# Kernel tuning notes

Measured on AMD Instinct MI355X. Metric: run time of the kernel, lower is better.

Reference implementation:

```python
import jax, jax.numpy as jnp
import numpy as np

N_NODES = 50000
N_EDGES = 800000
IN_CH = 128
HID_CH = 128
OUT_CH = 64
N_GRAPHS = 256


def setup_inputs() -> dict:
    key = jax.random.key(0)
    k1, k2, k3, k4, k5, k6, k7 = jax.random.split(key, 7)
    x = jax.random.normal(k1, (N_NODES, IN_CH), dtype=jnp.float32)
    edge_index = jax.random.randint(k2, (2, N_EDGES), 0, N_NODES, dtype=jnp.int64)
    batch = jnp.sort(jax.random.randint(k3, (N_NODES,), 0, N_GRAPHS, dtype=jnp.int64))
    # GCNConv params (glorot-ish scale) and Linear params
    W1 = jax.random.normal(k4, (IN_CH, HID_CH), dtype=jnp.float32) / np.sqrt(IN_CH)
    b1 = jnp.zeros((HID_CH,), dtype=jnp.float32)
    W2 = jax.random.normal(k5, (HID_CH, OUT_CH), dtype=jnp.float32) / np.sqrt(HID_CH)
    b2 = jax.random.normal(k6, (OUT_CH,), dtype=jnp.float32) * 0.01
    return {"x": x, "edge_index": edge_index, "batch": batch,
            "W1": W1, "b1": b1, "W2": W2, "b2": b2}


def _gcn_conv(x, edge_index, W, b):
    # PyG GCNConv: add self loops, symmetric normalization, linear transform,
    # gather-scale-scatter aggregation, bias.
    n = x.shape[0]
    loop = jnp.arange(n, dtype=edge_index.dtype)
    src = jnp.concatenate([edge_index[0], loop])  # message sources
    dst = jnp.concatenate([edge_index[1], loop])  # aggregation targets
    deg = jax.ops.segment_sum(jnp.ones_like(dst, dtype=x.dtype), dst, num_segments=n)
    dinv = jnp.where(deg > 0, jax.lax.rsqrt(deg), 0.0)
    norm = dinv[src] * dinv[dst]                  # [E+N]
    h = x @ W                                     # [N, hid] transform first (in >= hid)
    msg = h[src] * norm[:, None]                  # [E+N, hid] gather + scale
    agg = jax.ops.segment_sum(msg, dst, num_segments=n)  # scatter-add
    return agg + b


def reference(x, edge_index, batch, W1, b1, W2, b2):
    h = _gcn_conv(x, edge_index, W1, b1)
    h = jax.nn.relu(h)
    # dropout is identity in eval mode
    pooled = jax.ops.segment_max(h, batch, num_segments=N_GRAPHS)  # global max pool
    pooled = jnp.where(jnp.isfinite(pooled), pooled, 0.0)          # empty graphs -> 0
    out = jax.nn.relu(pooled @ W2 + b2)
    return out
```

## Files before the change

### kernel.cpp

```cpp
#include <hip/hip_runtime.h>

#define NN 50000
#define NE 800000
#define NG 256
#define NB 256
#define BW 196
#define NBIN 200
#define EPB 4000
#define PAD 16
#define CAP 4608
#define WT_STRIDE 136

typedef __attribute__((ext_vector_type(8))) short bf16x8;
typedef __attribute__((ext_vector_type(4))) float f32x4;
typedef __attribute__((ext_vector_type(2))) float f32x2;

static __device__ __forceinline__ unsigned short f2b(float f) {
    unsigned int u = __float_as_uint(f);
    return (unsigned short)((u + 0x7FFFu + ((u >> 16) & 1u)) >> 16);
}
static __device__ __forceinline__ unsigned char f2e4m3(float f) {
    int p = __builtin_amdgcn_cvt_pk_fp8_f32(f, 0.f, 0, false);
    return (unsigned char)(p & 0xFF);
}

__global__ __launch_bounds__(256) void k_bin(const int* __restrict__ src,
                                             const int* __restrict__ dst,
                                             int* __restrict__ bcur,
                                             unsigned int* __restrict__ ebuf) {
    __shared__ int lh[NB], gb[NB], lc[NB];
    int t = threadIdx.x;
    lh[t] = 0; lc[t] = 0;
    __syncthreads();
    int e0 = blockIdx.x * EPB;
    for (int i = e0 + t; i < e0 + EPB; i += 256)
        atomicAdd(&lh[(unsigned)dst[i] / BW], 1);
    __syncthreads();
    if (lh[t]) gb[t] = t * CAP + atomicAdd(&bcur[t * PAD], lh[t]);
    __syncthreads();
    for (int i = e0 + t; i < e0 + EPB; i += 256) {
        int d = dst[i];
        int b = (unsigned)d / BW;
        int r = atomicAdd(&lc[b], 1);
        ebuf[gb[b] + r] = ((unsigned)(d - b * BW) << 17) | (unsigned)src[i];
    }
}

__global__ __launch_bounds__(256) void k_sort(const unsigned int* __restrict__ ebuf,
                                              const int* __restrict__ bcur,
                                              int* __restrict__ csr_src,
                                              int* __restrict__ rowptr,
                                              int* __restrict__ deg,
                                              float* __restrict__ dinv) {
    __shared__ int hist[NB], off[NB], cur[NB];
    __shared__ int stage[CAP];
    const int t = threadIdx.x;
    const int b = blockIdx.x;
    const int cnt = bcur[b * PAD];
    const int ebeg = b * CAP;
    const int nbase = b * BW;
    hist[t] = 0; cur[t] = 0;
    __syncthreads();
    for (int i = t; i < cnt; i += 256)
        atomicAdd(&hist[ebuf[ebeg + i] >> 17], 1);
    __syncthreads();
    int v = hist[t];
    off[t] = v;
    __syncthreads();
    for (int o = 1; o < NB; o <<= 1) {
        int u = (t >= o) ? off[t - o] : 0;
        __syncthreads();
        off[t] += u;
        __syncthreads();
    }
    int ex = off[t] - v;
    int gn = nbase + t;
    if (t < BW && gn < NN) {
        rowptr[gn] = ebeg + ex;
        deg[gn] = v;
        dinv[gn] = rsqrtf((float)(v + 1));
    }
    __syncthreads();
    off[t] = ex;
    __syncthreads();
    for (int i = t; i < cnt; i += 256) {
        unsigned int p = ebuf[ebeg + i];
        int l = p >> 17;
        int r = atomicAdd(&cur[l], 1);
        stage[off[l] + r] = (int)(p & 0x1FFFFu);
    }
    __syncthreads();
    for (int i = t; i < cnt; i += 256)
        csr_src[ebeg + i] = stage[i];
}

__global__ __launch_bounds__(256) void k_gemm1(const float* __restrict__ x,
                                               const float* __restrict__ W,
                                               const float* __restrict__ dinv,
                                               unsigned char* __restrict__ h8) {
    __shared__ unsigned short Ws[128 * WT_STRIDE];
    const int tid = threadIdx.x;
#pragma unroll
    for (int p = 0; p < 64; ++p) {
        int g = p * 256 + tid;
        int k = g >> 7, n = g & 127;
        Ws[n * WT_STRIDE + k] = f2b(W[g]);
    }
    __syncthreads();
    const int w = tid >> 6, lane = tid & 63;
    const int q = lane >> 4, lid = lane & 15;
    const int m0 = blockIdx.x * 128 + w * 32;
    f32x4 acc[2][8];
#pragma unroll
    for (int rt = 0; rt < 2; ++rt)
#pragma unroll
        for (int jt = 0; jt < 8; ++jt) acc[rt][jt] = (f32x4){0.f, 0.f, 0.f, 0.f};

#pragma unroll
    for (int kt = 0; kt < 4; ++kt) {
        bf16x8 a[2];
#pragma unroll
        for (int rt = 0; rt < 2; ++rt) {
            int m = m0 + rt * 16 + lid;
            int k0 = kt * 32 + q * 8;
            float4 p0 = make_float4(0.f, 0.f, 0.f, 0.f), p1 = p0;
            if (m < NN) {
                p0 = *(const float4*)(x + (size_t)m * 128 + k0);
                p1 = *(const float4*)(x + (size_t)m * 128 + k0 + 4);
            }
            a[rt][0] = (short)f2b(p0.x); a[rt][1] = (short)f2b(p0.y);
            a[rt][2] = (short)f2b(p0.z); a[rt][3] = (short)f2b(p0.w);
            a[rt][4] = (short)f2b(p1.x); a[rt][5] = (short)f2b(p1.y);
            a[rt][6] = (short)f2b(p1.z); a[rt][7] = (short)f2b(p1.w);
        }
#pragma unroll
        for (int jt = 0; jt < 8; ++jt) {
            bf16x8 b = *(const bf16x8*)(Ws + (jt * 16 + lid) * WT_STRIDE + kt * 32 + q * 8);
            acc[0][jt] = __builtin_amdgcn_mfma_f32_16x16x32_bf16(a[0], b, acc[0][jt], 0, 0, 0);
            acc[1][jt] = __builtin_amdgcn_mfma_f32_16x16x32_bf16(a[1], b, acc[1][jt], 0, 0, 0);
        }
    }
#pragma unroll
    for (int rt = 0; rt < 2; ++rt)
#pragma unroll
        for (int reg = 0; reg < 4; ++reg) {
            int gr = m0 + rt * 16 + q * 4 + reg;
            if (gr < NN) {
                float di = dinv[gr];
#pragma unroll
                for (int jt = 0; jt < 8; ++jt)
                    h8[(size_t)gr * 128 + jt * 16 + lid] = f2e4m3(acc[rt][jt][reg] * di);
            }
        }
}

__global__ __launch_bounds__(256) void k_agg(const unsigned char* __restrict__ h8,
                                             const int* __restrict__ csr_src,
                                             const int* __restrict__ rowptr,
                                             const int* __restrict__ deg,
                                             const float* __restrict__ dinv,
                                             const float* __restrict__ b1,
                                             const int* __restrict__ batch,
                                             int* __restrict__ pooled) {
    const int tid = threadIdx.x;
    const int qg = tid >> 4, ql = tid & 15;
    const int n = blockIdx.x * 16 + qg;
    __shared__ float vals[16][128];
    __shared__ int bts[16];
    if (ql == 0) bts[qg] = batch[n];
    const float dd = dinv[n];
    const int beg = rowptr[n];
    const int end = beg + deg[n];
    const int c = ql * 8;
    float a[8];
#pragma unroll
    for (int j = 0; j < 8; ++j) a[j] = 0.f;
#pragma unroll 4
    for (int i = beg; i < end; ++i) {
        int s = csr_src[i];
        uint2 v = *(const uint2*)(h8 + (size_t)s * 128 + c);
        f32x2 f0 = __builtin_amdgcn_cvt_pk_f32_fp8((int)v.x, false);
        f32x2 f1 = __builtin_amdgcn_cvt_pk_f32_fp8((int)v.x, true);
        f32x2 f2 = __builtin_amdgcn_cvt_pk_f32_fp8((int)v.y, false);
        f32x2 f3 = __builtin_amdgcn_cvt_pk_f32_fp8((int)v.y, true);
        a[0] += f0.x; a[1] += f0.y; a[2] += f1.x; a[3] += f1.y;
        a[4] += f2.x; a[5] += f2.y; a[6] += f3.x; a[7] += f3.y;
    }
    {
        uint2 hv = *(const uint2*)(h8 + (size_t)n * 128 + c);
        f32x2 f0 = __builtin_amdgcn_cvt_pk_f32_fp8((int)hv.x, false);
        f32x2 f1 = __builtin_amdgcn_cvt_pk_f32_fp8((int)hv.x, true);
        f32x2 f2 = __builtin_amdgcn_cvt_pk_f32_fp8((int)hv.y, false);
        f32x2 f3 = __builtin_amdgcn_cvt_pk_f32_fp8((int)hv.y, true);
        float4 b0 = *(const float4*)(b1 + c);
        float4 b4 = *(const float4*)(b1 + c + 4);
        float r0 = fmaxf(dd * (a[0] + f0.x) + b0.x, 0.f);
        float r1 = fmaxf(dd * (a[1] + f0.y) + b0.y, 0.f);
        float r2 = fmaxf(dd * (a[2] + f1.x) + b0.z, 0.f);
        float r3 = fmaxf(dd * (a[3] + f1.y) + b0.w, 0.f);
        float r4 = fmaxf(dd * (a[4] + f2.x) + b4.x, 0.f);
        float r5 = fmaxf(dd * (a[5] + f2.y) + b4.y, 0.f);
        float r6 = fmaxf(dd * (a[6] + f3.x) + b4.z, 0.f);
        float r7 = fmaxf(dd * (a[7] + f3.y) + b4.w, 0.f);
        *(float4*)&vals[qg][c] = make_float4(r0, r1, r2, r3);
        *(float4*)&vals[qg][c + 4] = make_float4(r4, r5, r6, r7);
    }
    __syncthreads();
    if (tid < 128) {
        float m = vals[0][tid];
        int cur = bts[0];
#pragma unroll
        for (int ww = 1; ww < 16; ++ww) {
            if (bts[ww] != cur) {
                atomicMax(&pooled[cur * 128 + tid], __float_as_int(m));
                cur = bts[ww];
                m = vals[ww][tid];
            } else {
                m = fmaxf(m, vals[ww][tid]);
            }
        }
        atomicMax(&pooled[cur * 128 + tid], __float_as_int(m));
    }
}

__global__ __launch_bounds__(256) void k_gemm2(const float* __restrict__ pooled,
                                               const float* __restrict__ W2,
                                               const float* __restrict__ b2,
                                               float* __restrict__ out) {
    const int tid = threadIdx.x;
    const int row = blockIdx.x * 4 + (tid >> 6);
    const int col = tid & 63;
    const float* p = pooled + row * 128;
    float acc = b2[col];
    for (int k = 0; k < 128; ++k) acc += p[k] * W2[k * 64 + col];
    out[row * 64 + col] = fmaxf(acc, 0.f);
}

extern "C" void kernel_launch(void* const* d_in, const int* in_sizes, int n_in,
                              void* d_out, int out_size, void* d_ws, size_t ws_size,
                              hipStream_t stream) {
    const float* x     = (const float*)d_in[0];
    const int*   ei    = (const int*)d_in[1];
    const int*   batch = (const int*)d_in[2];
    const float* W1    = (const float*)d_in[3];
    const float* b1    = (const float*)d_in[4];
    const float* W2    = (const float*)d_in[5];
    const float* b2    = (const float*)d_in[6];
    float* out = (float*)d_out;

    int*   pooled  = (int*)d_ws;
    int*   bcur    = pooled + (size_t)NG * 128;
    int*   rowptr  = bcur + NB * PAD;
    int*   deg     = rowptr + NN;
    float* dinv    = (float*)(deg + NN);
    int*   csr_src = (int*)(dinv + NN);
    unsigned int* ebuf = (unsigned int*)(csr_src + (size_t)NB * CAP);
    unsigned char* h8  = (unsigned char*)(ebuf + (size_t)NB * CAP);

    size_t zbytes = ((size_t)NG * 128 + NB * PAD) * 4;
    hipMemsetAsync(d_ws, 0, zbytes, stream);

    const int* srcv = ei;
    const int* dstv = ei + NE;

    k_bin<<<NBIN, 256, 0, stream>>>(srcv, dstv, bcur, ebuf);
    k_sort<<<NB, 256, 0, stream>>>(ebuf, bcur, csr_src, rowptr, deg, dinv);
    k_gemm1<<<(NN + 127) / 128, 256, 0, stream>>>(x, W1, dinv, h8);
    k_agg<<<NN / 16, 256, 0, stream>>>(h8, csr_src, rowptr, deg, dinv, b1, batch, pooled);
    k_gemm2<<<NG / 4, 256, 0, stream>>>((const float*)pooled, W2, b2, out);
}
```

Before: 144.9 us.

## Split fp8 feature table into two channel halves and aggregate in two passes

The first GEMM now writes its fp8 output as two planar halves of 64 channels each, so each half-table is 3.2MB instead of 6.4MB. Aggregation runs twice, once per half, with each pass gathering 4 bytes per lane, in the hope that each half-table stays resident in cache during the random neighbour gathers. It also switches the CSR index loads to nontemporal. The cost is reading the CSR indices twice, an extra kernel launch, and twice the per-node overhead work.

```diff
diff --git a/kernel.cpp b/kernel.cpp
--- a/kernel.cpp
+++ b/kernel.cpp
@@ -10,6 +10,7 @@
 #define PAD 16
 #define CAP 4608
 #define WT_STRIDE 136
+#define PS ((size_t)NN * 64)
 
 typedef __attribute__((ext_vector_type(8))) short bf16x8;
 typedef __attribute__((ext_vector_type(4))) float f32x4;
@@ -149,77 +150,66 @@
                 float di = dinv[gr];
 #pragma unroll
                 for (int jt = 0; jt < 8; ++jt)
-                    h8[(size_t)gr * 128 + jt * 16 + lid] = f2e4m3(acc[rt][jt][reg] * di);
+                    h8[(size_t)(jt >> 2) * PS + (size_t)gr * 64 + ((jt & 3) << 4) + lid] =
+                        f2e4m3(acc[rt][jt][reg] * di);
             }
         }
 }
 
-__global__ __launch_bounds__(256) void k_agg(const unsigned char* __restrict__ h8,
+__global__ __launch_bounds__(256) void k_agg(const unsigned char* __restrict__ hp,
                                              const int* __restrict__ csr_src,
                                              const int* __restrict__ rowptr,
                                              const int* __restrict__ deg,
                                              const float* __restrict__ dinv,
                                              const float* __restrict__ b1,
                                              const int* __restrict__ batch,
-                                             int* __restrict__ pooled) {
+                                             int* __restrict__ pooled,
+                                             int cbase) {
     const int tid = threadIdx.x;
     const int qg = tid >> 4, ql = tid & 15;
     const int n = blockIdx.x * 16 + qg;
-    __shared__ float vals[16][128];
+    __shared__ float vals[16][64];
     __shared__ int bts[16];
     if (ql == 0) bts[qg] = batch[n];
     const float dd = dinv[n];
     const int beg = rowptr[n];
     const int end = beg + deg[n];
-    const int c = ql * 8;
-    float a[8];
-#pragma unroll
-    for (int j = 0; j < 8; ++j) a[j] = 0.f;
+    const int c = ql * 4;
+    float a0 = 0.f, a1 = 0.f, a2 = 0.f, a3 = 0.f;
 #pragma unroll 4
     for (int i = beg; i < end; ++i) {
-        int s = csr_src[i];
-        uint2 v = *(const uint2*)(h8 + (size_t)s * 128 + c);
-        f32x2 f0 = __builtin_amdgcn_cvt_pk_f32_fp8((int)v.x, false);
-        f32x2 f1 = __builtin_amdgcn_cvt_pk_f32_fp8((int)v.x, true);
-        f32x2 f2 = __builtin_amdgcn_cvt_pk_f32_fp8((int)v.y, false);
-        f32x2 f3 = __builtin_amdgcn_cvt_pk_f32_fp8((int)v.y, true);
-        a[0] += f0.x; a[1] += f0.y; a[2] += f1.x; a[3] += f1.y;
-        a[4] += f2.x; a[5] += f2.y; a[6] += f3.x; a[7] += f3.y;
+        int s = __builtin_nontemporal_load(csr_src + i);
+        unsigned int v = *(const unsigned int*)(hp + (size_t)s * 64 + c);
+        f32x2 f0 = __builtin_amdgcn_cvt_pk_f32_fp8((int)v, false);
+        f32x2 f1 = __builtin_amdgcn_cvt_pk_f32_fp8((int)v, true);
+        a0 += f0.x; a1 += f0.y; a2 += f1.x; a3 += f1.y;
     }
     {
-        uint2 hv = *(const uint2*)(h8 + (size_t)n * 128 + c);
-        f32x2 f0 = __builtin_amdgcn_cvt_pk_f32_fp8((int)hv.x, false);
-        f32x2 f1 = __builtin_amdgcn_cvt_pk_f32_fp8((int)hv.x, true);
-        f32x2 f2 = __builtin_amdgcn_cvt_pk_f32_fp8((int)hv.y, false);
-        f32x2 f3 = __builtin_amdgcn_cvt_pk_f32_fp8((int)hv.y, true);
-        float4 b0 = *(const float4*)(b1 + c);
-        float4 b4 = *(const float4*)(b1 + c + 4);
-        float r0 = fmaxf(dd * (a[0] + f0.x) + b0.x, 0.f);
-        float r1 = fmaxf(dd * (a[1] + f0.y) + b0.y, 0.f);
-        float r2 = fmaxf(dd * (a[2] + f1.x) + b0.z, 0.f);
-        float r3 = fmaxf(dd * (a[3] + f1.y) + b0.w, 0.f);
-        float r4 = fmaxf(dd * (a[4] + f2.x) + b4.x, 0.f);
-        float r5 = fmaxf(dd * (a[5] + f2.y) + b4.y, 0.f);
-        float r6 = fmaxf(dd * (a[6] + f3.x) + b4.z, 0.f);
-        float r7 = fmaxf(dd * (a[7] + f3.y) + b4.w, 0.f);
+        unsigned int hv = *(const unsigned int*)(hp + (size_t)n * 64 + c);
+        f32x2 f0 = __builtin_amdgcn_cvt_pk_f32_fp8((int)hv, false);
+        f32x2 f1 = __builtin_amdgcn_cvt_pk_f32_fp8((int)hv, true);
+        float4 bb = *(const float4*)(b1 + cbase + c);
+        float r0 = fmaxf(dd * (a0 + f0.x) + bb.x, 0.f);
+        float r1 = fmaxf(dd * (a1 + f0.y) + bb.y, 0.f);
+        float r2 = fmaxf(dd * (a2 + f1.x) + bb.z, 0.f);
+        float r3 = fmaxf(dd * (a3 + f1.y) + bb.w, 0.f);
         *(float4*)&vals[qg][c] = make_float4(r0, r1, r2, r3);
-        *(float4*)&vals[qg][c + 4] = make_float4(r4, r5, r6, r7);
-    }
-    __syncthreads();
-    if (tid < 128) {
+    }
+    __syncthreads();
+    if (tid < 64) {
         float m = vals[0][tid];
         int cur = bts[0];
 #pragma unroll
         for (int ww = 1; ww < 16; ++ww) {
             if (bts[ww] != cur) {
-                atomicMax(&pooled[cur * 128 + tid], __float_as_int(m));
+                atomicMax(&pooled[cur * 128 + cbase + tid], __float_as_int(m));
                 cur = bts[ww];
                 m = vals[ww][tid];
             } else {
                 m = fmaxf(m, vals[ww][tid]);
             }
         }
-        atomicMax(&pooled[cur * 128 + tid], __float_as_int(m));
+        atomicMax(&pooled[cur * 128 + cbase + tid], __float_as_int(m));
     }
 }
 
@@ -266,6 +256,7 @@
     k_bin<<<NBIN, 256, 0, stream>>>(srcv, dstv, bcur, ebuf);
     k_sort<<<NB, 256, 0, stream>>>(ebuf, bcur, csr_src, rowptr, deg, dinv);
     k_gemm1<<<(NN + 127) / 128, 256, 0, stream>>>(x, W1, dinv, h8);
-    k_agg<<<NN / 16, 256, 0, stream>>>(h8, csr_src, rowptr, deg, dinv, b1, batch, pooled);
+    k_agg<<<NN / 16, 256, 0, stream>>>(h8, csr_src, rowptr, deg, dinv, b1, batch, pooled, 0);
+    k_agg<<<NN / 16, 256, 0, stream>>>(h8 + PS, csr_src, rowptr, deg, dinv, b1, batch, pooled, 64);
     k_gemm2<<<NG / 4, 256, 0, stream>>>((const float*)pooled, W2, b2, out);
 }
```

Result: slower. 160.3 us (+10.6%).

## Merge edge binning and feature GEMM into one launch; apply source norm in aggregation

Applied to the files above, without the earlier changes.

The edge-binning kernel and the x@W1 GEMM kernel become one launch, with block index selecting the role. This lets the two independent stages run concurrently and removes a launch. Because the GEMM no longer waits for degrees, the dinv[src] scaling moves out of the GEMM epilogue and into the aggregation loop as an extra per-edge gather and FMA. Quantizing unscaled h to fp8 also changes the rounding behaviour slightly.

```diff
diff --git a/kernel.cpp b/kernel.cpp
--- a/kernel.cpp
+++ b/kernel.cpp
@@ -7,6 +7,7 @@
 #define BW 196
 #define NBIN 200
 #define EPB 4000
+#define NGEMM 391
 #define PAD 16
 #define CAP 4608
 #define WT_STRIDE 136
@@ -24,26 +25,88 @@
     return (unsigned char)(p & 0xFF);
 }
 
-__global__ __launch_bounds__(256) void k_bin(const int* __restrict__ src,
-                                             const int* __restrict__ dst,
-                                             int* __restrict__ bcur,
-                                             unsigned int* __restrict__ ebuf) {
-    __shared__ int lh[NB], gb[NB], lc[NB];
-    int t = threadIdx.x;
-    lh[t] = 0; lc[t] = 0;
-    __syncthreads();
-    int e0 = blockIdx.x * EPB;
-    for (int i = e0 + t; i < e0 + EPB; i += 256)
-        atomicAdd(&lh[(unsigned)dst[i] / BW], 1);
-    __syncthreads();
-    if (lh[t]) gb[t] = t * CAP + atomicAdd(&bcur[t * PAD], lh[t]);
-    __syncthreads();
-    for (int i = e0 + t; i < e0 + EPB; i += 256) {
-        int d = dst[i];
-        int b = (unsigned)d / BW;
-        int r = atomicAdd(&lc[b], 1);
-        ebuf[gb[b] + r] = ((unsigned)(d - b * BW) << 17) | (unsigned)src[i];
-    }
+__global__ __launch_bounds__(256) void k_front(const float* __restrict__ x,
+                                               const float* __restrict__ W,
+                                               unsigned char* __restrict__ h8,
+                                               const int* __restrict__ src,
+                                               const int* __restrict__ dst,
+                                               int* __restrict__ bcur,
+                                               unsigned int* __restrict__ ebuf) {
+    __shared__ unsigned short Ws[128 * WT_STRIDE];
+    const int tid = threadIdx.x;
+
+    if (blockIdx.x >= NGEMM) {
+        int* lh = (int*)Ws;
+        int* gb = lh + NB;
+        int* lc = gb + NB;
+        lh[tid] = 0; lc[tid] = 0;
+        __syncthreads();
+        int e0 = (blockIdx.x - NGEMM) * EPB;
+        for (int i = e0 + tid; i < e0 + EPB; i += 256)
+            atomicAdd(&lh[(unsigned)dst[i] / BW], 1);
+        __syncthreads();
+        if (lh[tid]) gb[tid] = tid * CAP + atomicAdd(&bcur[tid * PAD], lh[tid]);
+        __syncthreads();
+        for (int i = e0 + tid; i < e0 + EPB; i += 256) {
+            int d = dst[i];
+            int b = (unsigned)d / BW;
+            int r = atomicAdd(&lc[b], 1);
+            ebuf[gb[b] + r] = ((unsigned)(d - b * BW) << 17) | (unsigned)src[i];
+        }
+        return;
+    }
+
+#pragma unroll
+    for (int p = 0; p < 64; ++p) {
+        int g = p * 256 + tid;
+        int k = g >> 7, n = g & 127;
+        Ws[n * WT_STRIDE + k] = f2b(W[g]);
+    }
+    __syncthreads();
+    const int w = tid >> 6, lane = tid & 63;
+    const int q = lane >> 4, lid = lane & 15;
+    const int m0 = blockIdx.x * 128 + w * 32;
+    f32x4 acc[2][8];
+#pragma unroll
+    for (int rt = 0; rt < 2; ++rt)
+#pragma unroll
+        for (int jt = 0; jt < 8; ++jt) acc[rt][jt] = (f32x4){0.f, 0.f, 0.f, 0.f};
+
+#pragma unroll
+    for (int kt = 0; kt < 4; ++kt) {
+        bf16x8 a[2];
+#pragma unroll
+        for (int rt = 0; rt < 2; ++rt) {
+            int m = m0 + rt * 16 + lid;
+            int k0 = kt * 32 + q * 8;
+            float4 p0 = make_float4(0.f, 0.f, 0.f, 0.f), p1 = p0;
+            if (m < NN) {
+                p0 = *(const float4*)(x + (size_t)m * 128 + k0);
+                p1 = *(const float4*)(x + (size_t)m * 128 + k0 + 4);
+            }
+            a[rt][0] = (short)f2b(p0.x); a[rt][1] = (short)f2b(p0.y);
+            a[rt][2] = (short)f2b(p0.z); a[rt][3] = (short)f2b(p0.w);
+            a[rt][4] = (short)f2b(p1.x); a[rt][5] = (short)f2b(p1.y);
+            a[rt][6] = (short)f2b(p1.z); a[rt][7] = (short)f2b(p1.w);
+        }
+#pragma unroll
+        for (int jt = 0; jt < 8; ++jt) {
+            bf16x8 b = *(const bf16x8*)(Ws + (jt * 16 + lid) * WT_STRIDE + kt * 32 + q * 8);
+            acc[0][jt] = __builtin_amdgcn_mfma_f32_16x16x32_bf16(a[0], b, acc[0][jt], 0, 0, 0);
+            acc[1][jt] = __builtin_amdgcn_mfma_f32_16x16x32_bf16(a[1], b, acc[1][jt], 0, 0, 0);
+        }
+    }
+#pragma unroll
+    for (int rt = 0; rt < 2; ++rt)
+#pragma unroll
+        for (int reg = 0; reg < 4; ++reg) {
+            int gr = m0 + rt * 16 + q * 4 + reg;
+            if (gr < NN) {
+#pragma unroll
+                for (int jt = 0; jt < 8; ++jt)
+                    h8[(size_t)gr * 128 + jt * 16 + lid] = f2e4m3(acc[rt][jt][reg]);
+            }
+        }
 }
 
 __global__ __launch_bounds__(256) void k_sort(const unsigned int* __restrict__ ebuf,
@@ -92,66 +155,6 @@
     __syncthreads();
     for (int i = t; i < cnt; i += 256)
         csr_src[ebeg + i] = stage[i];
-}
-
-__global__ __launch_bounds__(256) void k_gemm1(const float* __restrict__ x,
-                                               const float* __restrict__ W,
-                                               const float* __restrict__ dinv,
-                                               unsigned char* __restrict__ h8) {
-    __shared__ unsigned short Ws[128 * WT_STRIDE];
-    const int tid = threadIdx.x;
-#pragma unroll
-    for (int p = 0; p < 64; ++p) {
-        int g = p * 256 + tid;
-        int k = g >> 7, n = g & 127;
-        Ws[n * WT_STRIDE + k] = f2b(W[g]);
-    }
-    __syncthreads();
-    const int w = tid >> 6, lane = tid & 63;
-    const int q = lane >> 4, lid = lane & 15;
-    const int m0 = blockIdx.x * 128 + w * 32;
-    f32x4 acc[2][8];
-#pragma unroll
-    for (int rt = 0; rt < 2; ++rt)
-#pragma unroll
-        for (int jt = 0; jt < 8; ++jt) acc[rt][jt] = (f32x4){0.f, 0.f, 0.f, 0.f};
-
-#pragma unroll
-    for (int kt = 0; kt < 4; ++kt) {
-        bf16x8 a[2];
-#pragma unroll
-        for (int rt = 0; rt < 2; ++rt) {
-            int m = m0 + rt * 16 + lid;
-            int k0 = kt * 32 + q * 8;
-            float4 p0 = make_float4(0.f, 0.f, 0.f, 0.f), p1 = p0;
-            if (m < NN) {
-                p0 = *(const float4*)(x + (size_t)m * 128 + k0);
-                p1 = *(const float4*)(x + (size_t)m * 128 + k0 + 4);
-            }
-            a[rt][0] = (short)f2b(p0.x); a[rt][1] = (short)f2b(p0.y);
-            a[rt][2] = (short)f2b(p0.z); a[rt][3] = (short)f2b(p0.w);
-            a[rt][4] = (short)f2b(p1.x); a[rt][5] = (short)f2b(p1.y);
-            a[rt][6] = (short)f2b(p1.z); a[rt][7] = (short)f2b(p1.w);
-        }
-#pragma unroll
-        for (int jt = 0; jt < 8; ++jt) {
-            bf16x8 b = *(const bf16x8*)(Ws + (jt * 16 + lid) * WT_STRIDE + kt * 32 + q * 8);
-            acc[0][jt] = __builtin_amdgcn_mfma_f32_16x16x32_bf16(a[0], b, acc[0][jt], 0, 0, 0);
-            acc[1][jt] = __builtin_amdgcn_mfma_f32_16x16x32_bf16(a[1], b, acc[1][jt], 0, 0, 0);
-        }
-    }
-#pragma unroll
-    for (int rt = 0; rt < 2; ++rt)
-#pragma unroll
-        for (int reg = 0; reg < 4; ++reg) {
-            int gr = m0 + rt * 16 + q * 4 + reg;
-            if (gr < NN) {
-                float di = dinv[gr];
-#pragma unroll
-                for (int jt = 0; jt < 8; ++jt)
-                    h8[(size_t)gr * 128 + jt * 16 + lid] = f2e4m3(acc[rt][jt][reg] * di);
-            }
-        }
 }
 
 __global__ __launch_bounds__(256) void k_agg(const unsigned char* __restrict__ h8,
@@ -178,13 +181,16 @@
 #pragma unroll 4
     for (int i = beg; i < end; ++i) {
         int s = csr_src[i];
+        float ds = dinv[s];
         uint2 v = *(const uint2*)(h8 + (size_t)s * 128 + c);
         f32x2 f0 = __builtin_amdgcn_cvt_pk_f32_fp8((int)v.x, false);
         f32x2 f1 = __builtin_amdgcn_cvt_pk_f32_fp8((int)v.x, true);
         f32x2 f2 = __builtin_amdgcn_cvt_pk_f32_fp8((int)v.y, false);
         f32x2 f3 = __builtin_amdgcn_cvt_pk_f32_fp8((int)v.y, true);
-        a[0] += f0.x; a[1] += f0.y; a[2] += f1.x; a[3] += f1.y;
-        a[4] += f2.x; a[5] += f2.y; a[6] += f3.x; a[7] += f3.y;
+        a[0] = fmaf(ds, f0.x, a[0]); a[1] = fmaf(ds, f0.y, a[1]);
+        a[2] = fmaf(ds, f1.x, a[2]); a[3] = fmaf(ds, f1.y, a[3]);
+        a[4] = fmaf(ds, f2.x, a[4]); a[5] = fmaf(ds, f2.y, a[5]);
+        a[6] = fmaf(ds, f3.x, a[6]); a[7] = fmaf(ds, f3.y, a[7]);
     }
     {
         uint2 hv = *(const uint2*)(h8 + (size_t)n * 128 + c);
@@ -194,14 +200,14 @@
         f32x2 f3 = __builtin_amdgcn_cvt_pk_f32_fp8((int)hv.y, true);
         float4 b0 = *(const float4*)(b1 + c);
         float4 b4 = *(const float4*)(b1 + c + 4);
-        float r0 = fmaxf(dd * (a[0] + f0.x) + b0.x, 0.f);
-        float r1 = fmaxf(dd * (a[1] + f0.y) + b0.y, 0.f);
-        float r2 = fmaxf(dd * (a[2] + f1.x) + b0.z, 0.f);
-        float r3 = fmaxf(dd * (a[3] + f1.y) + b0.w, 0.f);
-        float r4 = fmaxf(dd * (a[4] + f2.x) + b4.x, 0.f);
-        float r5 = fmaxf(dd * (a[5] + f2.y) + b4.y, 0.f);
-        float r6 = fmaxf(dd * (a[6] + f3.x) + b4.z, 0.f);
-        float r7 = fmaxf(dd * (a[7] + f3.y) + b4.w, 0.f);
+        float r0 = fmaxf(dd * fmaf(dd, f0.x, a[0]) + b0.x, 0.f);
+        float r1 = fmaxf(dd * fmaf(dd, f0.y, a[1]) + b0.y, 0.f);
+        float r2 = fmaxf(dd * fmaf(dd, f1.x, a[2]) + b0.z, 0.f);
+        float r3 = fmaxf(dd * fmaf(dd, f1.y, a[3]) + b0.w, 0.f);
+        float r4 = fmaxf(dd * fmaf(dd, f2.x, a[4]) + b4.x, 0.f);
+        float r5 = fmaxf(dd * fmaf(dd, f2.y, a[5]) + b4.y, 0.f);
+        float r6 = fmaxf(dd * fmaf(dd, f3.x, a[6]) + b4.z, 0.f);
+        float r7 = fmaxf(dd * fmaf(dd, f3.y, a[7]) + b4.w, 0.f);
         *(float4*)&vals[qg][c] = make_float4(r0, r1, r2, r3);
         *(float4*)&vals[qg][c + 4] = make_float4(r4, r5, r6, r7);
     }
@@ -263,9 +269,8 @@
     const int* srcv = ei;
     const int* dstv = ei + NE;
 
-    k_bin<<<NBIN, 256, 0, stream>>>(srcv, dstv, bcur, ebuf);
+    k_front<<<NGEMM + NBIN, 256, 0, stream>>>(x, W1, h8, srcv, dstv, bcur, ebuf);
     k_sort<<<NB, 256, 0, stream>>>(ebuf, bcur, csr_src, rowptr, deg, dinv);
-    k_gemm1<<<(NN + 127) / 128, 256, 0, stream>>>(x, W1, dinv, h8);
     k_agg<<<NN / 16, 256, 0, stream>>>(h8, csr_src, rowptr, deg, dinv, b1, batch, pooled);
     k_gemm2<<<NG / 4, 256, 0, stream>>>((const float*)pooled, W2, b2, out);
 }
```

New measurement: 137.7 us. -5.0%, faster.

## Fuse binning into GEMM launch and merge per-bucket sort with aggregation

Applied to the files above, without the earlier changes.

Degrees are now computed by a separate global-atomic kernel. Edge binning runs as extra blocks inside the first GEMM launch so the two overlap. The per-bucket counting sort and the neighbor aggregation with max-pooling are merged into one kernel with smaller buckets (25 nodes each), so the sorted sources stay in shared memory and the CSR array is never written to global memory. This removes two launches and a global round-trip, at the cost of global atomics on degree and a tight per-bucket capacity of 608 edges that could overflow on skewed inputs.

```diff
diff --git a/kernel.cpp b/kernel.cpp
--- a/kernel.cpp
+++ b/kernel.cpp
@@ -3,12 +3,13 @@
 #define NN 50000
 #define NE 800000
 #define NG 256
-#define NB 256
-#define BW 196
+#define NB 2000
+#define BW 25
 #define NBIN 200
 #define EPB 4000
+#define NGEMM 391
 #define PAD 16
-#define CAP 4608
+#define CAP 608
 #define WT_STRIDE 136
 
 typedef __attribute__((ext_vector_type(8))) short bf16x8;
@@ -24,82 +25,46 @@
     return (unsigned char)(p & 0xFF);
 }
 
-__global__ __launch_bounds__(256) void k_bin(const int* __restrict__ src,
-                                             const int* __restrict__ dst,
-                                             int* __restrict__ bcur,
-                                             unsigned int* __restrict__ ebuf) {
-    __shared__ int lh[NB], gb[NB], lc[NB];
-    int t = threadIdx.x;
-    lh[t] = 0; lc[t] = 0;
-    __syncthreads();
-    int e0 = blockIdx.x * EPB;
-    for (int i = e0 + t; i < e0 + EPB; i += 256)
-        atomicAdd(&lh[(unsigned)dst[i] / BW], 1);
-    __syncthreads();
-    if (lh[t]) gb[t] = t * CAP + atomicAdd(&bcur[t * PAD], lh[t]);
-    __syncthreads();
-    for (int i = e0 + t; i < e0 + EPB; i += 256) {
-        int d = dst[i];
-        int b = (unsigned)d / BW;
-        int r = atomicAdd(&lc[b], 1);
-        ebuf[gb[b] + r] = ((unsigned)(d - b * BW) << 17) | (unsigned)src[i];
-    }
-}
-
-__global__ __launch_bounds__(256) void k_sort(const unsigned int* __restrict__ ebuf,
-                                              const int* __restrict__ bcur,
-                                              int* __restrict__ csr_src,
-                                              int* __restrict__ rowptr,
-                                              int* __restrict__ deg,
-                                              float* __restrict__ dinv) {
-    __shared__ int hist[NB], off[NB], cur[NB];
-    __shared__ int stage[CAP];
-    const int t = threadIdx.x;
-    const int b = blockIdx.x;
-    const int cnt = bcur[b * PAD];
-    const int ebeg = b * CAP;
-    const int nbase = b * BW;
-    hist[t] = 0; cur[t] = 0;
-    __syncthreads();
-    for (int i = t; i < cnt; i += 256)
-        atomicAdd(&hist[ebuf[ebeg + i] >> 17], 1);
-    __syncthreads();
-    int v = hist[t];
-    off[t] = v;
-    __syncthreads();
-    for (int o = 1; o < NB; o <<= 1) {
-        int u = (t >= o) ? off[t - o] : 0;
-        __syncthreads();
-        off[t] += u;
-        __syncthreads();
-    }
-    int ex = off[t] - v;
-    int gn = nbase + t;
-    if (t < BW && gn < NN) {
-        rowptr[gn] = ebeg + ex;
-        deg[gn] = v;
-        dinv[gn] = rsqrtf((float)(v + 1));
-    }
-    __syncthreads();
-    off[t] = ex;
-    __syncthreads();
-    for (int i = t; i < cnt; i += 256) {
-        unsigned int p = ebuf[ebeg + i];
-        int l = p >> 17;
-        int r = atomicAdd(&cur[l], 1);
-        stage[off[l] + r] = (int)(p & 0x1FFFFu);
-    }
-    __syncthreads();
-    for (int i = t; i < cnt; i += 256)
-        csr_src[ebeg + i] = stage[i];
-}
-
-__global__ __launch_bounds__(256) void k_gemm1(const float* __restrict__ x,
+__global__ __launch_bounds__(256) void k_deg(const int* __restrict__ dst,
+                                             int* __restrict__ deg) {
+    int i0 = blockIdx.x * 256 + threadIdx.x;
+    for (int i = i0; i < NE; i += 256 * 256)
+        atomicAdd(&deg[dst[i]], 1);
+}
+
+__global__ __launch_bounds__(256) void k_front(const float* __restrict__ x,
                                                const float* __restrict__ W,
-                                               const float* __restrict__ dinv,
-                                               unsigned char* __restrict__ h8) {
-    __shared__ unsigned short Ws[128 * WT_STRIDE];
+                                               const int* __restrict__ deg,
+                                               unsigned char* __restrict__ h8,
+                                               const int* __restrict__ src,
+                                               const int* __restrict__ dst,
+                                               int* __restrict__ bcur,
+                                               unsigned int* __restrict__ ebuf) {
+    __shared__ __align__(16) unsigned short Ws[128 * WT_STRIDE];
     const int tid = threadIdx.x;
+
+    if (blockIdx.x >= NGEMM) {
+        int* lh = (int*)Ws;
+        int* gb = lh + NB;
+        int* lc = gb + NB;
+        for (int i = tid; i < NB; i += 256) { lh[i] = 0; lc[i] = 0; }
+        __syncthreads();
+        int e0 = (blockIdx.x - NGEMM) * EPB;
+        for (int i = e0 + tid; i < e0 + EPB; i += 256)
+            atomicAdd(&lh[(unsigned)dst[i] / BW], 1);
+        __syncthreads();
+        for (int i = tid; i < NB; i += 256)
+            if (lh[i]) gb[i] = i * CAP + atomicAdd(&bcur[i * PAD], lh[i]);
+        __syncthreads();
+        for (int i = e0 + tid; i < e0 + EPB; i += 256) {
+            int d = dst[i];
+            int b = (unsigned)d / BW;
+            int r = atomicAdd(&lc[b], 1);
+            ebuf[gb[b] + r] = ((unsigned)(d - b * BW) << 16) | (unsigned)src[i];
+        }
+        return;
+    }
+
 #pragma unroll
     for (int p = 0; p < 64; ++p) {
         int g = p * 256 + tid;
@@ -146,7 +111,7 @@
         for (int reg = 0; reg < 4; ++reg) {
             int gr = m0 + rt * 16 + q * 4 + reg;
             if (gr < NN) {
-                float di = dinv[gr];
+                float di = rsqrtf((float)(deg[gr] + 1));
 #pragma unroll
                 for (int jt = 0; jt < 8; ++jt)
                     h8[(size_t)gr * 128 + jt * 16 + lid] = f2e4m3(acc[rt][jt][reg] * di);
@@ -154,72 +119,103 @@
         }
 }
 
-__global__ __launch_bounds__(256) void k_agg(const unsigned char* __restrict__ h8,
-                                             const int* __restrict__ csr_src,
-                                             const int* __restrict__ rowptr,
-                                             const int* __restrict__ deg,
-                                             const float* __restrict__ dinv,
-                                             const float* __restrict__ b1,
-                                             const int* __restrict__ batch,
-                                             int* __restrict__ pooled) {
+__global__ __launch_bounds__(256) void k_sortagg(const unsigned int* __restrict__ ebuf,
+                                                 const int* __restrict__ bcur,
+                                                 const unsigned char* __restrict__ h8,
+                                                 const float* __restrict__ b1,
+                                                 const int* __restrict__ batch,
+                                                 int* __restrict__ pooled) {
+    __shared__ int hist[32], off[32], cur[32];
+    __shared__ int stage[CAP];
+    __shared__ float vals[16][132];
+    __shared__ int bts[16];
     const int tid = threadIdx.x;
-    const int qg = tid >> 4, ql = tid & 15;
-    const int n = blockIdx.x * 16 + qg;
-    __shared__ float vals[16][128];
-    __shared__ int bts[16];
-    if (ql == 0) bts[qg] = batch[n];
-    const float dd = dinv[n];
-    const int beg = rowptr[n];
-    const int end = beg + deg[n];
-    const int c = ql * 8;
-    float a[8];
-#pragma unroll
-    for (int j = 0; j < 8; ++j) a[j] = 0.f;
+    const int b = blockIdx.x;
+    const int cnt = bcur[b * PAD];
+    const int ebeg = b * CAP;
+    if (tid < 32) { hist[tid] = 0; cur[tid] = 0; }
+    __syncthreads();
+    for (int i = tid; i < cnt; i += 256)
+        atomicAdd(&hist[ebuf[ebeg + i] >> 16], 1);
+    __syncthreads();
+    if (tid == 0) {
+        int acc = 0;
+#pragma unroll
+        for (int l = 0; l < BW; ++l) { off[l] = acc; acc += hist[l]; }
+    }
+    __syncthreads();
+    for (int i = tid; i < cnt; i += 256) {
+        unsigned int p = ebuf[ebeg + i];
+        int l = p >> 16;
+        int r = atomicAdd(&cur[l], 1);
+        stage[off[l] + r] = (int)(p & 0xFFFFu);
+    }
+    __syncthreads();
+
+    const int g = tid >> 4, ql = tid & 15, c = ql * 8;
+#pragma unroll
+    for (int tile = 0; tile < 2; ++tile) {
+        const int l = tile * 16 + g;
+        const bool valid = (l < BW);
+        const int n = b * BW + l;
+        int dg = 0, beg = 0;
+        float dd = 0.f;
+        if (valid) {
+            dg = hist[l];
+            beg = off[l];
+            dd = rsqrtf((float)(dg + 1));
+            if (ql == 0) bts[g] = batch[n];
+        }
+        float a[8];
+#pragma unroll
+        for (int j = 0; j < 8; ++j) a[j] = 0.f;
 #pragma unroll 4
-    for (int i = beg; i < end; ++i) {
-        int s = csr_src[i];
-        uint2 v = *(const uint2*)(h8 + (size_t)s * 128 + c);
-        f32x2 f0 = __builtin_amdgcn_cvt_pk_f32_fp8((int)v.x, false);
-        f32x2 f1 = __builtin_amdgcn_cvt_pk_f32_fp8((int)v.x, true);
-        f32x2 f2 = __builtin_amdgcn_cvt_pk_f32_fp8((int)v.y, false);
-        f32x2 f3 = __builtin_amdgcn_cvt_pk_f32_fp8((int)v.y, true);
-        a[0] += f0.x; a[1] += f0.y; a[2] += f1.x; a[3] += f1.y;
-        a[4] += f2.x; a[5] += f2.y; a[6] += f3.x; a[7] += f3.y;
-    }
-    {
-        uint2 hv = *(const uint2*)(h8 + (size_t)n * 128 + c);
-        f32x2 f0 = __builtin_amdgcn_cvt_pk_f32_fp8((int)hv.x, false);
-        f32x2 f1 = __builtin_amdgcn_cvt_pk_f32_fp8((int)hv.x, true);
-        f32x2 f2 = __builtin_amdgcn_cvt_pk_f32_fp8((int)hv.y, false);
-        f32x2 f3 = __builtin_amdgcn_cvt_pk_f32_fp8((int)hv.y, true);
-        float4 b0 = *(const float4*)(b1 + c);
-        float4 b4 = *(const float4*)(b1 + c + 4);
-        float r0 = fmaxf(dd * (a[0] + f0.x) + b0.x, 0.f);
-        float r1 = fmaxf(dd * (a[1] + f0.y) + b0.y, 0.f);
-        float r2 = fmaxf(dd * (a[2] + f1.x) + b0.z, 0.f);
-        float r3 = fmaxf(dd * (a[3] + f1.y) + b0.w, 0.f);
-        float r4 = fmaxf(dd * (a[4] + f2.x) + b4.x, 0.f);
-        float r5 = fmaxf(dd * (a[5] + f2.y) + b4.y, 0.f);
-        float r6 = fmaxf(dd * (a[6] + f3.x) + b4.z, 0.f);
-        float r7 = fmaxf(dd * (a[7] + f3.y) + b4.w, 0.f);
-        *(float4*)&vals[qg][c] = make_float4(r0, r1, r2, r3);
-        *(float4*)&vals[qg][c + 4] = make_float4(r4, r5, r6, r7);
-    }
-    __syncthreads();
-    if (tid < 128) {
-        float m = vals[0][tid];
-        int cur = bts[0];
-#pragma unroll
-        for (int ww = 1; ww < 16; ++ww) {
-            if (bts[ww] != cur) {
-                atomicMax(&pooled[cur * 128 + tid], __float_as_int(m));
-                cur = bts[ww];
-                m = vals[ww][tid];
-            } else {
-                m = fmaxf(m, vals[ww][tid]);
+        for (int i = 0; i < dg; ++i) {
+            int s = stage[beg + i];
+            uint2 v = *(const uint2*)(h8 + (size_t)s * 128 + c);
+            f32x2 f0 = __builtin_amdgcn_cvt_pk_f32_fp8((int)v.x, false);
+            f32x2 f1 = __builtin_amdgcn_cvt_pk_f32_fp8((int)v.x, true);
+            f32x2 f2 = __builtin_amdgcn_cvt_pk_f32_fp8((int)v.y, false);
+            f32x2 f3 = __builtin_amdgcn_cvt_pk_f32_fp8((int)v.y, true);
+            a[0] += f0.x; a[1] += f0.y; a[2] += f1.x; a[3] += f1.y;
+            a[4] += f2.x; a[5] += f2.y; a[6] += f3.x; a[7] += f3.y;
+        }
+        if (valid) {
+            uint2 hv = *(const uint2*)(h8 + (size_t)n * 128 + c);
+            f32x2 f0 = __builtin_amdgcn_cvt_pk_f32_fp8((int)hv.x, false);
+            f32x2 f1 = __builtin_amdgcn_cvt_pk_f32_fp8((int)hv.x, true);
+            f32x2 f2 = __builtin_amdgcn_cvt_pk_f32_fp8((int)hv.y, false);
+            f32x2 f3 = __builtin_amdgcn_cvt_pk_f32_fp8((int)hv.y, true);
+            float4 b0 = *(const float4*)(b1 + c);
+            float4 b4 = *(const float4*)(b1 + c + 4);
+            float r0 = fmaxf(dd * (a[0] + f0.x) + b0.x, 0.f);
+            float r1 = fmaxf(dd * (a[1] + f0.y) + b0.y, 0.f);
+            float r2 = fmaxf(dd * (a[2] + f1.x) + b0.z, 0.f);
+            float r3 = fmaxf(dd * (a[3] + f1.y) + b0.w, 0.f);
+            float r4 = fmaxf(dd * (a[4] + f2.x) + b4.x, 0.f);
+            float r5 = fmaxf(dd * (a[5] + f2.y) + b4.y, 0.f);
+            float r6 = fmaxf(dd * (a[6] + f3.x) + b4.z, 0.f);
+            float r7 = fmaxf(dd * (a[7] + f3.y) + b4.w, 0.f);
+            *(float4*)&vals[g][c] = make_float4(r0, r1, r2, r3);
+            *(float4*)&vals[g][c + 4] = make_float4(r4, r5, r6, r7);
+        }
+        __syncthreads();
+        if (tid < 128) {
+            const int tcnt = (tile == 0) ? 16 : (BW - 16);
+            float m = vals[0][tid];
+            int curb = bts[0];
+            for (int ww = 1; ww < tcnt; ++ww) {
+                if (bts[ww] != curb) {
+                    atomicMax(&pooled[curb * 128 + tid], __float_as_int(m));
+                    curb = bts[ww];
+                    m = vals[ww][tid];
+                } else {
+                    m = fmaxf(m, vals[ww][tid]);
+                }
             }
-        }
-        atomicMax(&pooled[cur * 128 + tid], __float_as_int(m));
+            atomicMax(&pooled[curb * 128 + tid], __float_as_int(m));
+        }
+        __syncthreads();
     }
 }
 
@@ -250,22 +246,18 @@
 
     int*   pooled  = (int*)d_ws;
     int*   bcur    = pooled + (size_t)NG * 128;
-    int*   rowptr  = bcur + NB * PAD;
-    int*   deg     = rowptr + NN;
-    float* dinv    = (float*)(deg + NN);
-    int*   csr_src = (int*)(dinv + NN);
-    unsigned int* ebuf = (unsigned int*)(csr_src + (size_t)NB * CAP);
+    int*   deg     = bcur + (size_t)NB * PAD;
+    unsigned int* ebuf = (unsigned int*)(deg + NN);
     unsigned char* h8  = (unsigned char*)(ebuf + (size_t)NB * CAP);
 
-    size_t zbytes = ((size_t)NG * 128 + NB * PAD) * 4;
+    size_t zbytes = ((size_t)NG * 128 + (size_t)NB * PAD + NN) * 4;
     hipMemsetAsync(d_ws, 0, zbytes, stream);
 
     const int* srcv = ei;
     const int* dstv = ei + NE;
 
-    k_bin<<<NBIN, 256, 0, stream>>>(srcv, dstv, bcur, ebuf);
-    k_sort<<<NB, 256, 0, stream>>>(ebuf, bcur, csr_src, rowptr, deg, dinv);
-    k_gemm1<<<(NN + 127) / 128, 256, 0, stream>>>(x, W1, dinv, h8);
-    k_agg<<<NN / 16, 256, 0, stream>>>(h8, csr_src, rowptr, deg, dinv, b1, batch, pooled);
+    k_deg<<<256, 256, 0, stream>>>(dstv, deg);
+    k_front<<<NGEMM + NBIN, 256, 0, stream>>>(x, W1, deg, h8, srcv, dstv, bcur, ebuf);
+    k_sortagg<<<NB, 256, 0, stream>>>(ebuf, bcur, h8, b1, batch, pooled);
     k_gemm2<<<NG / 4, 256, 0, stream>>>((const float*)pooled, W2, b2, out);
 }
```

New measurement: 175.8 us. 21.3% more time.
